# Optimization experiments

Measured on AMD Instinct MI355X. Metric: run time of the kernel, lower is better.

The kernel has to match this reference:

```python
import jax, jax.numpy as jnp
import numpy as np

D_MODEL = 512
NHEAD = 8
WINDOW = 64


def setup_inputs() -> dict:
    key = jax.random.key(0)
    ks = jax.random.split(key, 5)
    d = D_MODEL
    x = jax.random.normal(ks[0], (8, 2048, d), dtype=jnp.float32)
    # nn.MultiheadAttention params: packed in-proj [3d, d] + bias [3d], out-proj [d, d] + bias [d]
    scale = 1.0 / np.sqrt(d)
    in_proj_w = jax.random.normal(ks[1], (3 * d, d), dtype=jnp.float32) * scale
    in_proj_b = jnp.zeros((3 * d,), dtype=jnp.float32)
    out_proj_w = jax.random.normal(ks[2], (d, d), dtype=jnp.float32) * scale
    out_proj_b = jnp.zeros((d,), dtype=jnp.float32)
    return {"x": x, "in_proj_w": in_proj_w, "in_proj_b": in_proj_b,
            "out_proj_w": out_proj_w, "out_proj_b": out_proj_b}


def reference(x, in_proj_w, in_proj_b, out_proj_w, out_proj_b):
    B, L, d = x.shape
    H = NHEAD
    dh = d // H
    # packed qkv projection (torch Linear: x @ W.T + b)
    qkv = jnp.einsum('bld,ed->ble', x, in_proj_w) + in_proj_b  # [B, L, 3d]
    q, k, v = jnp.split(qkv, 3, axis=-1)
    # split heads -> [B, H, L, dh]
    def heads(t):
        return t.reshape(B, L, H, dh).transpose(0, 2, 1, 3)
    q, k, v = heads(q), heads(k), heads(v)
    scores = jnp.einsum('bhqd,bhkd->bhqk', q, k) / jnp.sqrt(jnp.float32(dh))
    # banded mask: positions with |i-j| > window are masked out
    idx = jnp.arange(L)
    band = jnp.abs(idx[None, :] - idx[:, None]) > WINDOW  # [L, L] bool
    scores = jnp.where(band[None, None, :, :], jnp.float32(-jnp.inf), scores)
    p = jax.nn.softmax(scores, axis=-1)
    out = jnp.einsum('bhqk,bhkd->bhqd', p, v)  # [B, H, L, dh]
    out = out.transpose(0, 2, 1, 3).reshape(B, L, d)
    return jnp.einsum('bld,ed->ble', out, out_proj_w) + out_proj_b
```

## Files before the change

kernel.cpp:

```cpp
#include <hip/hip_runtime.h>

typedef __bf16 bf16x8 __attribute__((ext_vector_type(8)));
typedef unsigned short u16;
typedef unsigned short u16x8 __attribute__((ext_vector_type(8)));
typedef float f32x4 __attribute__((ext_vector_type(4)));

#define L_SEQ 2048
#define NQT   (L_SEQ / 128)

__device__ __forceinline__ float bf2f(u16 x) {
    unsigned u = ((unsigned)x) << 16;
    return __builtin_bit_cast(float, u);
}
__device__ __forceinline__ u16 f2bf(float f) {
    unsigned u = __builtin_bit_cast(unsigned, f);
    u += 0x7FFFu + ((u >> 16) & 1u);
    return (u16)(u >> 16);
}

__device__ __forceinline__ void gload_lds16(const u16* g, u16* l) {
    __builtin_amdgcn_global_load_lds(
        (const __attribute__((address_space(1))) void*)g,
        (__attribute__((address_space(3))) void*)l, 16, 0, 0);
}

__global__ void cvt_f32_bf16(const float* __restrict__ in, u16* __restrict__ out, int n8) {
    const int i = blockIdx.x * blockDim.x + threadIdx.x;
    if (i >= n8) return;
    const float4* p = reinterpret_cast<const float4*>(in) + (size_t)i * 2;
    const float4 a = p[0], b = p[1];
    u16x8 r;
    r[0] = f2bf(a.x); r[1] = f2bf(a.y); r[2] = f2bf(a.z); r[3] = f2bf(a.w);
    r[4] = f2bf(b.x); r[5] = f2bf(b.y); r[6] = f2bf(b.z); r[7] = f2bf(b.w);
    *(reinterpret_cast<u16x8*>(out) + i) = r;
}

template <bool OUT_BF16>
__launch_bounds__(256)
__global__ void gemm_bt_bias(const u16* __restrict__ A, const u16* __restrict__ W,
                             const float* __restrict__ bias, void* __restrict__ Cv,
                             int M, int N, int K) {
    __shared__ u16 As[2][128 * 64];
    __shared__ u16 Bs[2][128 * 64];

    const int tid   = threadIdx.x;
    const int lane  = tid & 63;
    const int wid   = tid >> 6;
    const int wm    = wid >> 1;
    const int wn    = wid & 1;
    const int row_l = lane & 15;
    const int grp   = lane >> 4;

    const int nwg  = gridDim.x * gridDim.y;
    const int hw   = blockIdx.y * gridDim.x + blockIdx.x;
    const int tile = (hw & 7) * (nwg >> 3) + (hw >> 3);
    const int m0 = (tile / gridDim.x) * 128;
    const int n0 = (tile % gridDim.x) * 128;

    const int srow = tid >> 3;
    const int scol = ((tid & 7) ^ (srow & 7)) * 8;
    const u16* gA = A + (size_t)(m0 + srow) * K + scol;
    const u16* gB = W + (size_t)(n0 + srow) * K + scol;

    f32x4 acc[4][4];
#pragma unroll
    for (int mi = 0; mi < 4; ++mi)
#pragma unroll
        for (int ni = 0; ni < 4; ++ni)
            acc[mi][ni] = (f32x4){0.f, 0.f, 0.f, 0.f};

    auto stage = [&](int buf, int kt) {
#pragma unroll
        for (int i = 0; i < 4; ++i) {
            gload_lds16(gA + (size_t)(i * 32) * K + kt * 64, &As[buf][i * 2048 + wid * 512]);
            gload_lds16(gB + (size_t)(i * 32) * K + kt * 64, &Bs[buf][i * 2048 + wid * 512]);
        }
    };

    auto compute = [&](int buf) {
#pragma unroll
        for (int kk = 0; kk < 2; ++kk) {
            bf16x8 a[4], b[4];
#pragma unroll
            for (int mi = 0; mi < 4; ++mi) {
                const int row = wm * 64 + mi * 16 + row_l;
                a[mi] = *reinterpret_cast<const bf16x8*>(
                    &As[buf][row * 64 + (((kk * 4 + grp) ^ (row & 7)) * 8)]);
            }
#pragma unroll
            for (int ni = 0; ni < 4; ++ni) {
                const int row = wn * 64 + ni * 16 + row_l;
                b[ni] = *reinterpret_cast<const bf16x8*>(
                    &Bs[buf][row * 64 + (((kk * 4 + grp) ^ (row & 7)) * 8)]);
            }
#pragma unroll
            for (int mi = 0; mi < 4; ++mi)
#pragma unroll
                for (int ni = 0; ni < 4; ++ni)
                    acc[mi][ni] = __builtin_amdgcn_mfma_f32_16x16x32_bf16(a[mi], b[ni], acc[mi][ni], 0, 0, 0);
        }
    };

    const int NT = K >> 6;
    stage(0, 0);
    __syncthreads();
    for (int t = 0; t < NT - 1; ++t) {
        const int cur = t & 1;
        stage(cur ^ 1, t + 1);
        compute(cur);
        __syncthreads();
    }
    compute((NT - 1) & 1);

#pragma unroll
    for (int ni = 0; ni < 4; ++ni) {
        const int col = n0 + wn * 64 + ni * 16 + row_l;
        const float bsf = bias[col];
#pragma unroll
        for (int mi = 0; mi < 4; ++mi) {
#pragma unroll
            for (int r = 0; r < 4; ++r) {
                const int rowm = m0 + wm * 64 + mi * 16 + grp * 4 + r;
                const float v = acc[mi][ni][r] + bsf;
                if (OUT_BF16)
                    ((u16*)Cv)[(size_t)rowm * N + col] = f2bf(v);
                else
                    ((float*)Cv)[(size_t)rowm * N + col] = v;
            }
        }
    }
}

__launch_bounds__(512, 4)
__global__ void local_attn(const u16* __restrict__ qkv, u16* __restrict__ att) {
    __shared__ __align__(16) u16 Ks[256 * 64];
    __shared__ __align__(16) u16 Vt[64 * 256];
    __shared__ __align__(16) u16 Pl[8][512];

    const int tid   = threadIdx.x;
    const int lane  = tid & 63;
    const int wv    = tid >> 6;
    const int row_l = lane & 15;
    const int grp   = lane >> 4;
    const int qt = blockIdx.x, h = blockIdx.y, b = blockIdx.z;
    const int q0b = qt * 128;
    const int kstart = q0b - 64;
    const size_t base = (size_t)b * L_SEQ * 1536;
    const bool edge = (qt == 0) || (qt == NQT - 1);

    {
        const int r0 = tid >> 3;
        const int c  = tid & 7;
#pragma unroll
        for (int i = 0; i < 4; ++i) {
            const int row  = i * 64 + r0;
            const int keyg = min(max(kstart + row, 0), L_SEQ - 1);
            const int cg   = c ^ (row & 7);
            gload_lds16(qkv + base + (size_t)keyg * 1536 + 512 + h * 64 + cg * 8,
                        &Ks[i * 4096 + wv * 512]);
        }
    }
    {
#pragma unroll
        for (int i = 0; i < 4; ++i) {
            const int idx  = i * 512 + tid;
            const int row  = idx >> 3;
            const int c8   = idx & 7;
            const int keyg = min(max(kstart + row, 0), L_SEQ - 1);
            const u16x8 vu = *reinterpret_cast<const u16x8*>(
                qkv + base + (size_t)keyg * 1536 + 1024 + h * 64 + c8 * 8);
#pragma unroll
            for (int e = 0; e < 8; ++e) {
                const int d = c8 * 8 + e;
                Vt[d * 256 + (((row >> 3) ^ (d & 7)) * 8) + (row & 7)] = vu[e];
            }
        }
    }

    const int qrow_g = q0b + wv * 16 + row_l;
    const u16* qp = qkv + base + (size_t)qrow_g * 1536 + h * 64;
    const bf16x8 qf0 = *reinterpret_cast<const bf16x8*>(qp + grp * 8);
    const bf16x8 qf1 = *reinterpret_cast<const bf16x8*>(qp + 32 + grp * 8);

    __syncthreads();

    float m_r = -1e30f, l_r = 0.f;
    f32x4 acc[4];
#pragma unroll
    for (int ds = 0; ds < 4; ++ds) acc[ds] = (f32x4){0.f, 0.f, 0.f, 0.f};
    u16* Pw = Pl[wv];

    auto do_chunk = [&](int c, bool bandLo, bool bandHi, bool half, bool rng) {
        const int kcL = wv * 16 + 32 * c;
        const int kcG = kstart + kcL;
        const int nf = half ? 1 : 2;

        f32x4 s[2];
#pragma unroll
        for (int f = 0; f < 2; ++f) {
            if (f >= nf) break;
            const int rr = kcL + 16 * f + row_l;
            const bf16x8 ka = *reinterpret_cast<const bf16x8*>(
                &Ks[rr * 64 + ((grp ^ (rr & 7)) * 8)]);
            const bf16x8 kb = *reinterpret_cast<const bf16x8*>(
                &Ks[rr * 64 + (((grp + 4) ^ (rr & 7)) * 8)]);
            f32x4 z = (f32x4){0.f, 0.f, 0.f, 0.f};
            z = __builtin_amdgcn_mfma_f32_16x16x32_bf16(ka, qf0, z, 0, 0, 0);
            z = __builtin_amdgcn_mfma_f32_16x16x32_bf16(kb, qf1, z, 0, 0, 0);
            s[f] = z;
        }

        float p[2][4];
        float cmax = -1e30f;
#pragma unroll
        for (int f = 0; f < 2; ++f) {
            if (f >= nf) break;
#pragma unroll
            for (int r = 0; r < 4; ++r) {
                const int k = 16 * f + grp * 4 + r;
                bool ok = true;
                if (bandLo) ok = ok && (k >= row_l);
                if (bandHi) ok = ok && (k <= row_l);
                if (rng) { const int kg = kcG + k; ok = ok && (kg >= 0) && (kg < L_SEQ); }
                const float sv = ok ? s[f][r] * 0.125f : -1e30f;
                p[f][r] = sv;
                cmax = fmaxf(cmax, sv);
            }
        }
        cmax = fmaxf(cmax, __shfl_xor(cmax, 16, 64));
        cmax = fmaxf(cmax, __shfl_xor(cmax, 32, 64));
        const float mn  = fmaxf(m_r, cmax);
        const float scl = __expf(m_r - mn);
        m_r = mn;
        float lsum = 0.f;
#pragma unroll
        for (int f = 0; f < 2; ++f) {
            if (f >= nf) break;
#pragma unroll
            for (int r = 0; r < 4; ++r) {
                const float pv = (p[f][r] <= -1e29f) ? 0.f : __expf(p[f][r] - mn);
                p[f][r] = pv;
                lsum += pv;
            }
        }
        lsum += __shfl_xor(lsum, 16, 64);
        lsum += __shfl_xor(lsum, 32, 64);
        l_r = l_r * scl + lsum;

        float scl4[4];
#pragma unroll
        for (int r = 0; r < 4; ++r) scl4[r] = __shfl(scl, grp * 4 + r, 64);
#pragma unroll
        for (int ds = 0; ds < 4; ++ds)
#pragma unroll
            for (int r = 0; r < 4; ++r) acc[ds][r] *= scl4[r];

#pragma unroll
        for (int f = 0; f < 2; ++f)
#pragma unroll
            for (int r = 0; r < 4; ++r) {
                const int k = 16 * f + grp * 4 + r;
                const int slot = (k >> 3) ^ ((row_l >> 1) & 3);
                const float pv = (f < nf) ? p[f][r] : 0.f;
                Pw[row_l * 32 + slot * 8 + (k & 7)] = f2bf(pv);
            }
        const bf16x8 pa = *reinterpret_cast<const bf16x8*>(
            &Pw[row_l * 32 + ((grp ^ ((row_l >> 1) & 3)) * 8)]);

        int k0 = kcL + grp * 8;
        if (half) k0 = min(k0, 248);
#pragma unroll
        for (int ds = 0; ds < 4; ++ds) {
            const int d = ds * 16 + row_l;
            const bf16x8 vf = *reinterpret_cast<const bf16x8*>(
                &Vt[d * 256 + (((k0 >> 3) ^ (d & 7)) * 8)]);
            acc[ds] = __builtin_amdgcn_mfma_f32_16x16x32_bf16(pa, vf, acc[ds], 0, 0, 0);
        }
    };

    if (!edge) {
        do_chunk(0, true,  false, false, false);
        do_chunk(1, false, false, false, false);
        do_chunk(2, false, false, false, false);
        do_chunk(3, false, false, false, false);
        do_chunk(4, false, true,  true,  false);
    } else {
        const int kw = kstart + wv * 16;
        if (kw       > -32 && kw       < L_SEQ) do_chunk(0, true,  false, false, true);
        if (kw + 32  > -32 && kw + 32  < L_SEQ) do_chunk(1, false, false, false, true);
        if (kw + 64  > -32 && kw + 64  < L_SEQ) do_chunk(2, false, false, false, true);
        if (kw + 96  > -32 && kw + 96  < L_SEQ) do_chunk(3, false, false, false, true);
        if (kw + 128 > -32 && kw + 128 < L_SEQ) do_chunk(4, false, true,  true,  true);
    }

    const float inv = 1.f / l_r;
    float inv4[4];
#pragma unroll
    for (int r = 0; r < 4; ++r) inv4[r] = __shfl(inv, grp * 4 + r, 64);
    const int qg = q0b + wv * 16 + grp * 4;
#pragma unroll
    for (int r = 0; r < 4; ++r)
#pragma unroll
        for (int ds = 0; ds < 4; ++ds)
            att[(size_t)(b * L_SEQ + qg + r) * 512 + h * 64 + ds * 16 + row_l] =
                f2bf(acc[ds][r] * inv4[r]);
}

extern "C" void kernel_launch(void* const* d_in, const int* in_sizes, int n_in,
                              void* d_out, int out_size, void* d_ws, size_t ws_size,
                              hipStream_t stream) {
    const float* x     = (const float*)d_in[0];
    const float* w_in  = (const float*)d_in[1];
    const float* b_in  = (const float*)d_in[2];
    const float* w_out = (const float*)d_in[3];
    const float* b_out = (const float*)d_in[4];
    float* out = (float*)d_out;

    const int B = 8, L = L_SEQ;
    const int M = B * L;

    u16* qkv   = (u16*)d_ws;
    u16* att   = qkv   + (size_t)M * 1536;
    u16* x_bf  = att   + (size_t)M * 512;
    u16* wi_bf = x_bf  + (size_t)M * 512;
    u16* wo_bf = wi_bf + (size_t)1536 * 512;

    {
        const int nx = M * 512 / 8;
        cvt_f32_bf16<<<(nx + 255) / 256, 256, 0, stream>>>(x, x_bf, nx);
        const int nwi = 1536 * 512 / 8;
        cvt_f32_bf16<<<(nwi + 255) / 256, 256, 0, stream>>>(w_in, wi_bf, nwi);
        const int nwo = 512 * 512 / 8;
        cvt_f32_bf16<<<(nwo + 255) / 256, 256, 0, stream>>>(w_out, wo_bf, nwo);
    }

    gemm_bt_bias<true><<<dim3(1536 / 128, M / 128), dim3(256), 0, stream>>>(
        x_bf, wi_bf, b_in, qkv, M, 1536, 512);

    local_attn<<<dim3(NQT, 8, B), dim3(512), 0, stream>>>(qkv, att);

    gemm_bt_bias<false><<<dim3(512 / 128, M / 128), dim3(256), 0, stream>>>(
        att, wo_bf, b_out, out, M, 512, 512);
}
```

Before: 95.51 us.

## Add 256x256-tile QKV GEMM with 4-stage LDS pipeline and merge conversion kernels

Merges the three fp32-to-bf16 conversion launches into one kernel that picks its source by global index, removing two launches. Replaces the 128x128 QKV projection GEMM with a new 512-thread kernel using 256x256 output tiles, BK=32, a 4-slot direct-to-LDS load pipeline with manual vmcnt waits, swizzled LDS layout, XCD-aware tile remapping, and setprio around the MFMA loop. The larger tiles raise data reuse per block but give only 384 blocks and higher register pressure (128 accumulator floats per thread). The output stores are scattered per-element bf16 writes.

```diff
diff --git a/kernel.cpp b/kernel.cpp
--- a/kernel.cpp
+++ b/kernel.cpp
@@ -24,15 +24,125 @@
         (__attribute__((address_space(3))) void*)l, 16, 0, 0);
 }
 
-__global__ void cvt_f32_bf16(const float* __restrict__ in, u16* __restrict__ out, int n8) {
-    const int i = blockIdx.x * blockDim.x + threadIdx.x;
-    if (i >= n8) return;
-    const float4* p = reinterpret_cast<const float4*>(in) + (size_t)i * 2;
+__global__ void cvt_all(const float* __restrict__ x, const float* __restrict__ wi,
+                        const float* __restrict__ wo, u16* __restrict__ xo,
+                        u16* __restrict__ wio, u16* __restrict__ woo,
+                        int nx8, int nwi8, int nwo8) {
+    int i = blockIdx.x * blockDim.x + threadIdx.x;
+    const float* src; u16* dst;
+    if (i < nx8) { src = x; dst = xo; }
+    else if (i < nx8 + nwi8) { i -= nx8; src = wi; dst = wio; }
+    else if (i < nx8 + nwi8 + nwo8) { i -= nx8 + nwi8; src = wo; dst = woo; }
+    else return;
+    const float4* p = reinterpret_cast<const float4*>(src) + (size_t)i * 2;
     const float4 a = p[0], b = p[1];
     u16x8 r;
     r[0] = f2bf(a.x); r[1] = f2bf(a.y); r[2] = f2bf(a.z); r[3] = f2bf(a.w);
     r[4] = f2bf(b.x); r[5] = f2bf(b.y); r[6] = f2bf(b.z); r[7] = f2bf(b.w);
-    *(reinterpret_cast<u16x8*>(out) + i) = r;
+    *(reinterpret_cast<u16x8*>(dst) + i) = r;
+}
+
+__launch_bounds__(512, 2)
+__global__ void gemm_qkv(const u16* __restrict__ A, const u16* __restrict__ W,
+                         const float* __restrict__ bias, u16* __restrict__ C,
+                         int M, int N, int K) {
+    __shared__ u16 As[4][256 * 32];
+    __shared__ u16 Bs[4][256 * 32];
+
+    const int tid   = threadIdx.x;
+    const int lane  = tid & 63;
+    const int wid   = tid >> 6;
+    const int wm    = wid >> 2;
+    const int wn    = wid & 3;
+    const int row_l = lane & 15;
+    const int grp   = lane >> 4;
+
+    const int nwg  = gridDim.x * gridDim.y;
+    const int hw   = blockIdx.y * gridDim.x + blockIdx.x;
+    const int tile = (hw & 7) * (nwg >> 3) + (hw >> 3);
+    const int m0 = (tile / gridDim.x) * 256;
+    const int n0 = (tile % gridDim.x) * 256;
+
+    const int row_st = tid >> 2;
+    const int c_st   = tid & 3;
+    const int swz    = (c_st ^ ((row_st >> 1) & 3)) * 8;
+    const u16* gA = A + (size_t)(m0 + row_st) * K + swz;
+    const u16* gB = W + (size_t)(n0 + row_st) * K + swz;
+    u16* lA = &As[0][0] + wid * 512;
+    u16* lB = &Bs[0][0] + wid * 512;
+
+    f32x4 acc[8][4];
+#pragma unroll
+    for (int mi = 0; mi < 8; ++mi)
+#pragma unroll
+        for (int ni = 0; ni < 4; ++ni)
+            acc[mi][ni] = (f32x4){0.f, 0.f, 0.f, 0.f};
+
+    auto stage = [&](int slot, int kt) {
+#pragma unroll
+        for (int i = 0; i < 2; ++i) {
+            gload_lds16(gA + (size_t)(i * 128) * K + kt * 32, lA + slot * 8192 + i * 4096);
+            gload_lds16(gB + (size_t)(i * 128) * K + kt * 32, lB + slot * 8192 + i * 4096);
+        }
+    };
+
+    const int rchunk = (grp ^ ((row_l >> 1) & 3)) * 8;
+
+    auto compute = [&](int slot) {
+        bf16x8 a[8], b[4];
+#pragma unroll
+        for (int mi = 0; mi < 8; ++mi)
+            a[mi] = *reinterpret_cast<const bf16x8*>(
+                &As[slot][(wm * 128 + mi * 16 + row_l) * 32 + rchunk]);
+#pragma unroll
+        for (int ni = 0; ni < 4; ++ni)
+            b[ni] = *reinterpret_cast<const bf16x8*>(
+                &Bs[slot][(wn * 64 + ni * 16 + row_l) * 32 + rchunk]);
+        __builtin_amdgcn_s_setprio(1);
+#pragma unroll
+        for (int mi = 0; mi < 8; ++mi)
+#pragma unroll
+            for (int ni = 0; ni < 4; ++ni)
+                acc[mi][ni] = __builtin_amdgcn_mfma_f32_16x16x32_bf16(a[mi], b[ni], acc[mi][ni], 0, 0, 0);
+        __builtin_amdgcn_s_setprio(0);
+    };
+
+    const int NT = K >> 5;
+    stage(0, 0); stage(1, 1); stage(2, 2);
+
+    for (int c = 0; c < NT - 3; ++c) {
+        asm volatile("s_waitcnt vmcnt(8)" ::: "memory");
+        __builtin_amdgcn_s_barrier();
+        asm volatile("" ::: "memory");
+        stage((c + 3) & 3, c + 3);
+        compute(c & 3);
+    }
+    asm volatile("s_waitcnt vmcnt(8)" ::: "memory");
+    __builtin_amdgcn_s_barrier();
+    asm volatile("" ::: "memory");
+    compute((NT - 3) & 3);
+    asm volatile("s_waitcnt vmcnt(4)" ::: "memory");
+    __builtin_amdgcn_s_barrier();
+    asm volatile("" ::: "memory");
+    compute((NT - 2) & 3);
+    asm volatile("s_waitcnt vmcnt(0)" ::: "memory");
+    __builtin_amdgcn_s_barrier();
+    asm volatile("" ::: "memory");
+    compute((NT - 1) & 3);
+
+#pragma unroll
+    for (int ni = 0; ni < 4; ++ni) {
+        const int col = n0 + wn * 64 + ni * 16 + row_l;
+        const float bsf = bias[col];
+#pragma unroll
+        for (int mi = 0; mi < 8; ++mi) {
+#pragma unroll
+            for (int r = 0; r < 4; ++r) {
+                const int rowm = m0 + wm * 128 + mi * 16 + grp * 4 + r;
+                C[(size_t)rowm * N + col] = f2bf(acc[mi][ni][r] + bsf);
+            }
+        }
+    }
 }
 
 template <bool OUT_BF16>
@@ -325,16 +435,14 @@
     u16* wi_bf = x_bf  + (size_t)M * 512;
     u16* wo_bf = wi_bf + (size_t)1536 * 512;
 
-    {
-        const int nx = M * 512 / 8;
-        cvt_f32_bf16<<<(nx + 255) / 256, 256, 0, stream>>>(x, x_bf, nx);
-        const int nwi = 1536 * 512 / 8;
-        cvt_f32_bf16<<<(nwi + 255) / 256, 256, 0, stream>>>(w_in, wi_bf, nwi);
-        const int nwo = 512 * 512 / 8;
-        cvt_f32_bf16<<<(nwo + 255) / 256, 256, 0, stream>>>(w_out, wo_bf, nwo);
-    }
-
-    gemm_bt_bias<true><<<dim3(1536 / 128, M / 128), dim3(256), 0, stream>>>(
+    const int nx8  = M * 512 / 8;
+    const int nwi8 = 1536 * 512 / 8;
+    const int nwo8 = 512 * 512 / 8;
+    const int ncvt = nx8 + nwi8 + nwo8;
+    cvt_all<<<(ncvt + 255) / 256, 256, 0, stream>>>(x, w_in, w_out, x_bf, wi_bf, wo_bf,
+                                                    nx8, nwi8, nwo8);
+
+    gemm_qkv<<<dim3(1536 / 256, M / 256), dim3(512), 0, stream>>>(
         x_bf, wi_bf, b_in, qkv, M, 1536, 512);
 
     local_attn<<<dim3(NQT, 8, B), dim3(512), 0, stream>>>(qkv, att);
```

New measurement: 103.7 us. 1.09x slower.

## Use triple-buffered K32 GEMM ring pipeline and fuse conversion launches

Applied to the files above, without the earlier changes.

Rewrites the bf16 GEMM to use a three-stage LDS ring with K-tiles of 32. Waits use explicit vmcnt counts and a single barrier per step, so global-to-LDS loads for tile t+2 overlap compute on tile t. MFMA issue is wrapped in s_setprio, and launch bounds now request 3 waves per SIMD. The three f32-to-bf16 conversion kernels are merged into one launch to cut launch overhead. The risks are more loop iterations with fewer MFMAs per barrier and a swizzle scheme that must stay correct and free of bank conflicts.

```diff
diff --git a/kernel.cpp b/kernel.cpp
--- a/kernel.cpp
+++ b/kernel.cpp
@@ -24,24 +24,31 @@
         (__attribute__((address_space(3))) void*)l, 16, 0, 0);
 }
 
-__global__ void cvt_f32_bf16(const float* __restrict__ in, u16* __restrict__ out, int n8) {
-    const int i = blockIdx.x * blockDim.x + threadIdx.x;
-    if (i >= n8) return;
-    const float4* p = reinterpret_cast<const float4*>(in) + (size_t)i * 2;
+__global__ void cvt_all(const float* __restrict__ x, const float* __restrict__ wi,
+                        const float* __restrict__ wo, u16* __restrict__ xo,
+                        u16* __restrict__ wio, u16* __restrict__ woo,
+                        int nx8, int nwi8, int nwo8) {
+    int i = blockIdx.x * blockDim.x + threadIdx.x;
+    const float* src; u16* dst;
+    if (i < nx8) { src = x; dst = xo; }
+    else if (i < nx8 + nwi8) { i -= nx8; src = wi; dst = wio; }
+    else if (i < nx8 + nwi8 + nwo8) { i -= nx8 + nwi8; src = wo; dst = woo; }
+    else return;
+    const float4* p = reinterpret_cast<const float4*>(src) + (size_t)i * 2;
     const float4 a = p[0], b = p[1];
     u16x8 r;
     r[0] = f2bf(a.x); r[1] = f2bf(a.y); r[2] = f2bf(a.z); r[3] = f2bf(a.w);
     r[4] = f2bf(b.x); r[5] = f2bf(b.y); r[6] = f2bf(b.z); r[7] = f2bf(b.w);
-    *(reinterpret_cast<u16x8*>(out) + i) = r;
+    *(reinterpret_cast<u16x8*>(dst) + i) = r;
 }
 
 template <bool OUT_BF16>
-__launch_bounds__(256)
-__global__ void gemm_bt_bias(const u16* __restrict__ A, const u16* __restrict__ W,
-                             const float* __restrict__ bias, void* __restrict__ Cv,
-                             int M, int N, int K) {
-    __shared__ u16 As[2][128 * 64];
-    __shared__ u16 Bs[2][128 * 64];
+__launch_bounds__(256, 3)
+__global__ void gemm_ring(const u16* __restrict__ A, const u16* __restrict__ W,
+                          const float* __restrict__ bias, void* __restrict__ Cv,
+                          int M, int N, int K) {
+    __shared__ u16 As[3][128 * 32];
+    __shared__ u16 Bs[3][128 * 32];
 
     const int tid   = threadIdx.x;
     const int lane  = tid & 63;
@@ -57,8 +64,8 @@
     const int m0 = (tile / gridDim.x) * 128;
     const int n0 = (tile % gridDim.x) * 128;
 
-    const int srow = tid >> 3;
-    const int scol = ((tid & 7) ^ (srow & 7)) * 8;
+    const int srow = tid >> 2;
+    const int scol = ((tid & 3) ^ ((tid >> 3) & 3)) * 8;
     const u16* gA = A + (size_t)(m0 + srow) * K + scol;
     const u16* gB = W + (size_t)(n0 + srow) * K + scol;
 
@@ -71,46 +78,48 @@
 
     auto stage = [&](int buf, int kt) {
 #pragma unroll
-        for (int i = 0; i < 4; ++i) {
-            gload_lds16(gA + (size_t)(i * 32) * K + kt * 64, &As[buf][i * 2048 + wid * 512]);
-            gload_lds16(gB + (size_t)(i * 32) * K + kt * 64, &Bs[buf][i * 2048 + wid * 512]);
+        for (int i = 0; i < 2; ++i) {
+            gload_lds16(gA + (size_t)(i * 64) * K + kt * 32, &As[buf][i * 2048 + wid * 512]);
+            gload_lds16(gB + (size_t)(i * 64) * K + kt * 32, &Bs[buf][i * 2048 + wid * 512]);
         }
     };
 
+    const int rchunk = (grp ^ ((row_l >> 1) & 3)) * 8;
+
     auto compute = [&](int buf) {
-#pragma unroll
-        for (int kk = 0; kk < 2; ++kk) {
-            bf16x8 a[4], b[4];
-#pragma unroll
-            for (int mi = 0; mi < 4; ++mi) {
-                const int row = wm * 64 + mi * 16 + row_l;
-                a[mi] = *reinterpret_cast<const bf16x8*>(
-                    &As[buf][row * 64 + (((kk * 4 + grp) ^ (row & 7)) * 8)]);
-            }
-#pragma unroll
-            for (int ni = 0; ni < 4; ++ni) {
-                const int row = wn * 64 + ni * 16 + row_l;
-                b[ni] = *reinterpret_cast<const bf16x8*>(
-                    &Bs[buf][row * 64 + (((kk * 4 + grp) ^ (row & 7)) * 8)]);
-            }
-#pragma unroll
-            for (int mi = 0; mi < 4; ++mi)
-#pragma unroll
-                for (int ni = 0; ni < 4; ++ni)
-                    acc[mi][ni] = __builtin_amdgcn_mfma_f32_16x16x32_bf16(a[mi], b[ni], acc[mi][ni], 0, 0, 0);
-        }
+        bf16x8 a[4], b[4];
+#pragma unroll
+        for (int mi = 0; mi < 4; ++mi)
+            a[mi] = *reinterpret_cast<const bf16x8*>(
+                &As[buf][(wm * 64 + mi * 16 + row_l) * 32 + rchunk]);
+#pragma unroll
+        for (int ni = 0; ni < 4; ++ni)
+            b[ni] = *reinterpret_cast<const bf16x8*>(
+                &Bs[buf][(wn * 64 + ni * 16 + row_l) * 32 + rchunk]);
+        __builtin_amdgcn_s_setprio(1);
+#pragma unroll
+        for (int mi = 0; mi < 4; ++mi)
+#pragma unroll
+            for (int ni = 0; ni < 4; ++ni)
+                acc[mi][ni] = __builtin_amdgcn_mfma_f32_16x16x32_bf16(a[mi], b[ni], acc[mi][ni], 0, 0, 0);
+        __builtin_amdgcn_s_setprio(0);
     };
 
-    const int NT = K >> 6;
+    const int NT = K >> 5;
     stage(0, 0);
-    __syncthreads();
-    for (int t = 0; t < NT - 1; ++t) {
-        const int cur = t & 1;
-        stage(cur ^ 1, t + 1);
+    stage(1, 1);
+    int cur = 0;
+    for (int t = 0; t < NT; ++t) {
+        if (t == NT - 1) asm volatile("s_waitcnt vmcnt(0)" ::: "memory");
+        else             asm volatile("s_waitcnt vmcnt(4)" ::: "memory");
+        __builtin_amdgcn_s_barrier();
+        if (t + 2 < NT) {
+            int st = cur + 2; if (st >= 3) st -= 3;
+            stage(st, t + 2);
+        }
         compute(cur);
-        __syncthreads();
-    }
-    compute((NT - 1) & 1);
+        cur = cur + 1; if (cur >= 3) cur = 0;
+    }
 
 #pragma unroll
     for (int ni = 0; ni < 4; ++ni) {
@@ -325,20 +334,18 @@
     u16* wi_bf = x_bf  + (size_t)M * 512;
     u16* wo_bf = wi_bf + (size_t)1536 * 512;
 
-    {
-        const int nx = M * 512 / 8;
-        cvt_f32_bf16<<<(nx + 255) / 256, 256, 0, stream>>>(x, x_bf, nx);
-        const int nwi = 1536 * 512 / 8;
-        cvt_f32_bf16<<<(nwi + 255) / 256, 256, 0, stream>>>(w_in, wi_bf, nwi);
-        const int nwo = 512 * 512 / 8;
-        cvt_f32_bf16<<<(nwo + 255) / 256, 256, 0, stream>>>(w_out, wo_bf, nwo);
-    }
-
-    gemm_bt_bias<true><<<dim3(1536 / 128, M / 128), dim3(256), 0, stream>>>(
+    const int nx8  = M * 512 / 8;
+    const int nwi8 = 1536 * 512 / 8;
+    const int nwo8 = 512 * 512 / 8;
+    const int ncvt = nx8 + nwi8 + nwo8;
+    cvt_all<<<(ncvt + 255) / 256, 256, 0, stream>>>(x, w_in, w_out, x_bf, wi_bf, wo_bf,
+                                                    nx8, nwi8, nwo8);
+
+    gemm_ring<true><<<dim3(1536 / 128, M / 128), dim3(256), 0, stream>>>(
         x_bf, wi_bf, b_in, qkv, M, 1536, 512);
 
     local_attn<<<dim3(NQT, 8, B), dim3(512), 0, stream>>>(qkv, att);
 
-    gemm_bt_bias<false><<<dim3(512 / 128, M / 128), dim3(256), 0, stream>>>(
+    gemm_ring<false><<<dim3(512 / 128, M / 128), dim3(256), 0, stream>>>(
         att, wo_bf, b_out, out, M, 512, 512);
 }
```

New measurement: 90.77 us. -5.0%, faster.
